# Optimization experiments

Measured on AMD Instinct MI355X. Metric: run time of the kernel, lower is better.

## Reference

```python
import jax, jax.numpy as jnp
import numpy as np

KH, KW = 3, 3
STRIDE = (1, 1)


def setup_inputs() -> dict:
    key = jax.random.key(0)
    k1, k2, k3 = jax.random.split(key, 3)
    N, C, H, W = 16, 128, 64, 64
    O = 128
    x = jax.random.normal(k1, (N, C, H, W), dtype=jnp.float32)
    # Flat weight layout [O, C*KH*KW], matching torch reshape of [O,C,KH,KW]
    weight = jax.random.normal(k2, (O, C * KH * KW), dtype=jnp.float32) * 0.02
    bias = jax.random.normal(k3, (O, 1), dtype=jnp.float32) * 0.02
    return {"x": x, "weight": weight, "bias": bias}


def reference(x, weight, bias):
    O = weight.shape[0]
    C = x.shape[1]
    # [O, C*KH*KW] -> [O, C, KH, KW]; flattening order (C major, then kh, kw)
    # matches the module's unfold/permute im2col layout.
    w4 = weight.reshape(O, C, KH, KW)
    out = jax.lax.conv_general_dilated(
        x, w4,
        window_strides=STRIDE,
        padding='VALID',
        dimension_numbers=('NCHW', 'OIHW', 'NCHW'),
    )
    return out + bias.reshape(1, O, 1, 1)
```

## Files before the change

kernel.cpp:

```cpp
#include <hip/hip_runtime.h>
#include <stdint.h>

#define AS_G __attribute__((address_space(1)))
#define AS_L __attribute__((address_space(3)))

typedef __bf16 bf16x8 __attribute__((ext_vector_type(8)));
typedef float  f32x4  __attribute__((ext_vector_type(4)));

static constexpr int NIMG = 16, CIN = 128, H = 64, W = 64, OCH = 128;
static constexpr int HO = 62, WO = 62;
static constexpr int PIX = HO * WO;
static constexpr int M_TOT = NIMG * PIX;
static constexpr int K_TOT = CIN * 9;
static constexpr int BM = 64, BK = 64;
static constexpr int KSTEPS = K_TOT / BK;
static constexpr int NWG = M_TOT / BM;
static constexpr int SLOT = 24576;
static constexpr int LDS_BYTES = 3 * SLOT;

__device__ __forceinline__ unsigned short f2bf(float f) {
    union { float f; uint32_t u; } v; v.f = f;
    uint32_t u = v.u;
    return (unsigned short)((u + 0x7FFFu + ((u >> 16) & 1u)) >> 16);
}

__global__ __launch_bounds__(256) void prep_kernel(const float* __restrict__ x,
                                                   const float* __restrict__ wsrc,
                                                   unsigned short* __restrict__ xt,
                                                   unsigned short* __restrict__ bpd) {
    __shared__ float lds[CIN][W + 4];
    if (blockIdx.x < NIMG * H) {
        const int n   = blockIdx.x >> 6;
        const int h   = blockIdx.x & 63;
        const int tid = threadIdx.x;
        {
            const int c  = tid >> 1;
            const int w0 = (tid & 1) * 32;
            const float* src = x + (((size_t)(n * CIN + c) * H + h) * W + w0);
            #pragma unroll
            for (int j = 0; j < 8; ++j) {
                float4 v = *reinterpret_cast<const float4*>(src + j * 4);
                *reinterpret_cast<float4*>(&lds[c][w0 + j * 4]) = v;
            }
        }
        __syncthreads();
        {
            const int w  = tid >> 2;
            const int c0 = (tid & 3) * 32;
            unsigned short* dst = xt + (((size_t)(n * H + h) * W + w) * CIN + c0);
            uint32_t pk[16];
            #pragma unroll
            for (int j = 0; j < 16; ++j) {
                uint32_t lo = f2bf(lds[c0 + 2 * j][w]);
                uint32_t hi = f2bf(lds[c0 + 2 * j + 1][w]);
                pk[j] = lo | (hi << 16);
            }
            #pragma unroll
            for (int j = 0; j < 4; ++j) {
                *reinterpret_cast<uint4*>(dst + j * 8) =
                    make_uint4(pk[4 * j], pk[4 * j + 1], pk[4 * j + 2], pk[4 * j + 3]);
            }
        }
    } else {
        int tid = (blockIdx.x - NIMG * H) * 256 + threadIdx.x;
        if (tid < OCH * K_TOT) {
            int o  = tid / K_TOT;
            int kp = tid - o * K_TOT;
            int t  = kp >> 7;
            int c  = kp & 127;
            bpd[tid] = f2bf(wsrc[o * K_TOT + c * 9 + t]);
        }
    }
}

__global__ __launch_bounds__(256) void gemm_kernel(const unsigned short* __restrict__ xt,
                                                   const unsigned short* __restrict__ bp,
                                                   const float* __restrict__ bias,
                                                   float* __restrict__ out) {
    extern __shared__ char lds[];
    const int tid  = threadIdx.x;
    const int wv   = tid >> 6;
    const int lane = tid & 63;

    const int orig = blockIdx.x;
    const int xcd  = orig & 7;
    const int idx  = orig >> 3;
    const int wg   = (xcd == 0 ? 0 : 121 + (xcd - 1) * 120) + idx;
    const int m0   = wg * BM;

    const int csel = ((lane & 7) ^ (lane >> 3)) * 8;
    int aBase[2], bBase[4];
    #pragma unroll
    for (int i = 0; i < 2; ++i) {
        int row = (wv * 2 + i) * 8 + (lane >> 3);
        int m = m0 + row;
        int n  = m / PIX;
        int r  = m - n * PIX;
        int y  = r / WO;
        int xx = r - y * WO;
        aBase[i] = ((n * H + y) * W + xx) * CIN;
    }
    #pragma unroll
    for (int i = 0; i < 4; ++i)
        bBase[i] = ((wv * 4 + i) * 8 + (lane >> 3)) * K_TOT;

    auto stage = [&](char* dst, int step) {
        const int t  = step >> 1;
        const int c0 = (step & 1) * 64;
        const int tapoff = (t / 3) * (W * CIN) + (t % 3) * CIN + c0;
        const int kb = step * BK;
        #pragma unroll
        for (int i = 0; i < 2; ++i)
            __builtin_amdgcn_global_load_lds(
                (AS_G unsigned int*)(xt + aBase[i] + tapoff + csel),
                (AS_L unsigned int*)(dst + (wv * 2 + i) * 1024), 16, 0, 0);
        #pragma unroll
        for (int i = 0; i < 4; ++i)
            __builtin_amdgcn_global_load_lds(
                (AS_G unsigned int*)(bp + bBase[i] + kb + csel),
                (AS_L unsigned int*)(dst + 8192 + (wv * 4 + i) * 1024), 16, 0, 0);
    };

    const int wr = wv >> 1, wc = wv & 1;
    const int lr = lane & 15, lq = lane >> 4;
    const int aRow = (wr * 32 + lr) * 128;
    const int bRow = (wc * 64 + lr) * 128;
    int colx[2];
    #pragma unroll
    for (int ks = 0; ks < 2; ++ks)
        colx[ks] = (ks * 64 + lq * 16) ^ ((lane & 7) << 4);

    f32x4 acc[2][4];
    #pragma unroll
    for (int a = 0; a < 2; ++a)
        #pragma unroll
        for (int b = 0; b < 4; ++b)
            acc[a][b] = (f32x4){0.f, 0.f, 0.f, 0.f};

    auto compute = [&](const char* base) {
        #pragma unroll
        for (int ks = 0; ks < 2; ++ks) {
            bf16x8 af[2], bfr[4];
            #pragma unroll
            for (int mi = 0; mi < 2; ++mi)
                af[mi] = *(const bf16x8*)(base + aRow + mi * 2048 + colx[ks]);
            #pragma unroll
            for (int ni = 0; ni < 4; ++ni)
                bfr[ni] = *(const bf16x8*)(base + 8192 + bRow + ni * 2048 + colx[ks]);
            __builtin_amdgcn_s_setprio(1);
            #pragma unroll
            for (int mi = 0; mi < 2; ++mi)
                #pragma unroll
                for (int ni = 0; ni < 4; ++ni)
                    acc[mi][ni] = __builtin_amdgcn_mfma_f32_16x16x32_bf16(
                        bfr[ni], af[mi], acc[mi][ni], 0, 0, 0);
            __builtin_amdgcn_s_setprio(0);
        }
    };

    char* b0 = lds;
    char* b1 = lds + SLOT;
    char* b2 = lds + 2 * SLOT;
    stage(b0, 0);
    stage(b1, 1);
    for (int t = 0; t < KSTEPS - 2; ++t) {
        stage(b2, t + 2);
        asm volatile("s_waitcnt vmcnt(12)" ::: "memory");
        __builtin_amdgcn_s_barrier();
        __builtin_amdgcn_sched_barrier(0);
        compute(b0);
        asm volatile("s_waitcnt lgkmcnt(0)" ::: "memory");
        __builtin_amdgcn_s_barrier();
        __builtin_amdgcn_sched_barrier(0);
        char* tmp = b0; b0 = b1; b1 = b2; b2 = tmp;
    }
    asm volatile("s_waitcnt vmcnt(6)" ::: "memory");
    __builtin_amdgcn_s_barrier();
    __builtin_amdgcn_sched_barrier(0);
    compute(b0);
    asm volatile("s_waitcnt vmcnt(0)" ::: "memory");
    __builtin_amdgcn_s_barrier();
    __builtin_amdgcn_sched_barrier(0);
    compute(b1);

    f32x4 bv[4];
    #pragma unroll
    for (int ni = 0; ni < 4; ++ni)
        bv[ni] = *(const f32x4*)(bias + wc * 64 + ni * 16 + lq * 4);
    #pragma unroll
    for (int mi = 0; mi < 2; ++mi) {
        int m = m0 + wr * 32 + mi * 16 + lr;
        int n  = m / PIX;
        int r  = m - n * PIX;
        int y  = r / WO;
        int xx = r - y * WO;
        float* ob = out + (size_t)n * OCH * PIX + y * WO + xx;
        #pragma unroll
        for (int ni = 0; ni < 4; ++ni)
            #pragma unroll
            for (int j = 0; j < 4; ++j) {
                int o = wc * 64 + ni * 16 + lq * 4 + j;
                ob[(size_t)o * PIX] = acc[mi][ni][j] + bv[ni][j];
            }
    }
}

extern "C" void kernel_launch(void* const* d_in, const int* in_sizes, int n_in,
                              void* d_out, int out_size, void* d_ws, size_t ws_size,
                              hipStream_t stream) {
    const float* x    = (const float*)d_in[0];
    const float* wsrc = (const float*)d_in[1];
    const float* bias = (const float*)d_in[2];
    float* out = (float*)d_out;
    unsigned short* xt = (unsigned short*)d_ws;
    unsigned short* bp = xt + (size_t)NIMG * H * W * CIN;
    prep_kernel<<<dim3(NIMG * H + (OCH * K_TOT + 255) / 256), dim3(256), 0, stream>>>(
        x, wsrc, xt, bp);
    gemm_kernel<<<dim3(NWG), dim3(256), LDS_BYTES, stream>>>(xt, bp, bias, out);
}
```

Baseline: 44.29 us.

## Enlarge GEMM block tile to 256 rows with 512 threads per block

Grows the implicit-GEMM M tile from 64 to 256 pixels and the block from 4 to 8 waves, giving each wave a 64x64 output tile (4x4 MFMA accumulators). Weight tiles staged into LDS are now reused across four times as many pixels, and each LDS fragment read feeds more MFMAs. It adds bounds clamping for the partial last tile and rebalances the XCD block remap for 241 blocks. The cost is one large block per CU with a bigger LDS footprint, fewer total blocks than CUs, and more accumulator registers per wave.

```diff
diff --git a/kernel.cpp b/kernel.cpp
--- a/kernel.cpp
+++ b/kernel.cpp
@@ -12,10 +12,12 @@
 static constexpr int PIX = HO * WO;
 static constexpr int M_TOT = NIMG * PIX;
 static constexpr int K_TOT = CIN * 9;
-static constexpr int BM = 64, BK = 64;
+static constexpr int BM = 256, BK = 64;
 static constexpr int KSTEPS = K_TOT / BK;
-static constexpr int NWG = M_TOT / BM;
-static constexpr int SLOT = 24576;
+static constexpr int NWG = (M_TOT + BM - 1) / BM;
+static constexpr int ASZ = BM * BK * 2;
+static constexpr int BSZ = OCH * BK * 2;
+static constexpr int SLOT = ASZ + BSZ;
 static constexpr int LDS_BYTES = 3 * SLOT;
 
 __device__ __forceinline__ unsigned short f2bf(float f) {
@@ -73,10 +75,10 @@
     }
 }
 
-__global__ __launch_bounds__(256) void gemm_kernel(const unsigned short* __restrict__ xt,
-                                                   const unsigned short* __restrict__ bp,
-                                                   const float* __restrict__ bias,
-                                                   float* __restrict__ out) {
+__global__ __launch_bounds__(512, 1) void gemm_kernel(const unsigned short* __restrict__ xt,
+                                                      const unsigned short* __restrict__ bp,
+                                                      const float* __restrict__ bias,
+                                                      float* __restrict__ out) {
     extern __shared__ char lds[];
     const int tid  = threadIdx.x;
     const int wv   = tid >> 6;
@@ -85,24 +87,25 @@
     const int orig = blockIdx.x;
     const int xcd  = orig & 7;
     const int idx  = orig >> 3;
-    const int wg   = (xcd == 0 ? 0 : 121 + (xcd - 1) * 120) + idx;
+    const int wg   = (xcd == 0 ? 0 : 31 + (xcd - 1) * 30) + idx;
     const int m0   = wg * BM;
 
-    const int csel = ((lane & 7) ^ (lane >> 3)) * 8;
-    int aBase[2], bBase[4];
-    #pragma unroll
-    for (int i = 0; i < 2; ++i) {
-        int row = (wv * 2 + i) * 8 + (lane >> 3);
-        int m = m0 + row;
+    const int csel = ((tid & 7) ^ ((tid >> 3) & 7)) * 8;
+    int aBase[4];
+    #pragma unroll
+    for (int p = 0; p < 4; ++p) {
+        int row = p * 64 + (tid >> 3);
+        int m = m0 + row; if (m >= M_TOT) m = M_TOT - 1;
         int n  = m / PIX;
         int r  = m - n * PIX;
         int y  = r / WO;
         int xx = r - y * WO;
-        aBase[i] = ((n * H + y) * W + xx) * CIN;
-    }
-    #pragma unroll
-    for (int i = 0; i < 4; ++i)
-        bBase[i] = ((wv * 4 + i) * 8 + (lane >> 3)) * K_TOT;
+        aBase[p] = ((n * H + y) * W + xx) * CIN;
+    }
+    int bBase[2];
+    #pragma unroll
+    for (int p = 0; p < 2; ++p)
+        bBase[p] = (p * 64 + (tid >> 3)) * K_TOT;
 
     auto stage = [&](char* dst, int step) {
         const int t  = step >> 1;
@@ -110,29 +113,29 @@
         const int tapoff = (t / 3) * (W * CIN) + (t % 3) * CIN + c0;
         const int kb = step * BK;
         #pragma unroll
-        for (int i = 0; i < 2; ++i)
+        for (int p = 0; p < 4; ++p)
             __builtin_amdgcn_global_load_lds(
-                (AS_G unsigned int*)(xt + aBase[i] + tapoff + csel),
-                (AS_L unsigned int*)(dst + (wv * 2 + i) * 1024), 16, 0, 0);
-        #pragma unroll
-        for (int i = 0; i < 4; ++i)
+                (AS_G unsigned int*)(xt + aBase[p] + tapoff + csel),
+                (AS_L unsigned int*)(dst + p * 8192 + wv * 1024), 16, 0, 0);
+        #pragma unroll
+        for (int p = 0; p < 2; ++p)
             __builtin_amdgcn_global_load_lds(
-                (AS_G unsigned int*)(bp + bBase[i] + kb + csel),
-                (AS_L unsigned int*)(dst + 8192 + (wv * 4 + i) * 1024), 16, 0, 0);
+                (AS_G unsigned int*)(bp + bBase[p] + kb + csel),
+                (AS_L unsigned int*)(dst + ASZ + p * 8192 + wv * 1024), 16, 0, 0);
     };
 
     const int wr = wv >> 1, wc = wv & 1;
     const int lr = lane & 15, lq = lane >> 4;
-    const int aRow = (wr * 32 + lr) * 128;
-    const int bRow = (wc * 64 + lr) * 128;
+    const int aRow = (wr * 64 + lr) * 128;
+    const int bRow = ASZ + (wc * 64 + lr) * 128;
     int colx[2];
     #pragma unroll
     for (int ks = 0; ks < 2; ++ks)
         colx[ks] = (ks * 64 + lq * 16) ^ ((lane & 7) << 4);
 
-    f32x4 acc[2][4];
-    #pragma unroll
-    for (int a = 0; a < 2; ++a)
+    f32x4 acc[4][4];
+    #pragma unroll
+    for (int a = 0; a < 4; ++a)
         #pragma unroll
         for (int b = 0; b < 4; ++b)
             acc[a][b] = (f32x4){0.f, 0.f, 0.f, 0.f};
@@ -140,16 +143,16 @@
     auto compute = [&](const char* base) {
         #pragma unroll
         for (int ks = 0; ks < 2; ++ks) {
-            bf16x8 af[2], bfr[4];
-            #pragma unroll
-            for (int mi = 0; mi < 2; ++mi)
+            bf16x8 af[4], bfr[4];
+            #pragma unroll
+            for (int mi = 0; mi < 4; ++mi)
                 af[mi] = *(const bf16x8*)(base + aRow + mi * 2048 + colx[ks]);
             #pragma unroll
             for (int ni = 0; ni < 4; ++ni)
-                bfr[ni] = *(const bf16x8*)(base + 8192 + bRow + ni * 2048 + colx[ks]);
+                bfr[ni] = *(const bf16x8*)(base + bRow + ni * 2048 + colx[ks]);
             __builtin_amdgcn_s_setprio(1);
             #pragma unroll
-            for (int mi = 0; mi < 2; ++mi)
+            for (int mi = 0; mi < 4; ++mi)
                 #pragma unroll
                 for (int ni = 0; ni < 4; ++ni)
                     acc[mi][ni] = __builtin_amdgcn_mfma_f32_16x16x32_bf16(
@@ -188,20 +191,22 @@
     for (int ni = 0; ni < 4; ++ni)
         bv[ni] = *(const f32x4*)(bias + wc * 64 + ni * 16 + lq * 4);
     #pragma unroll
-    for (int mi = 0; mi < 2; ++mi) {
-        int m = m0 + wr * 32 + mi * 16 + lr;
-        int n  = m / PIX;
-        int r  = m - n * PIX;
-        int y  = r / WO;
-        int xx = r - y * WO;
-        float* ob = out + (size_t)n * OCH * PIX + y * WO + xx;
-        #pragma unroll
-        for (int ni = 0; ni < 4; ++ni)
-            #pragma unroll
-            for (int j = 0; j < 4; ++j) {
-                int o = wc * 64 + ni * 16 + lq * 4 + j;
-                ob[(size_t)o * PIX] = acc[mi][ni][j] + bv[ni][j];
-            }
+    for (int mi = 0; mi < 4; ++mi) {
+        int m = m0 + wr * 64 + mi * 16 + lr;
+        if (m < M_TOT) {
+            int n  = m / PIX;
+            int r  = m - n * PIX;
+            int y  = r / WO;
+            int xx = r - y * WO;
+            float* ob = out + (size_t)n * OCH * PIX + y * WO + xx;
+            #pragma unroll
+            for (int ni = 0; ni < 4; ++ni)
+                #pragma unroll
+                for (int j = 0; j < 4; ++j) {
+                    int o = wc * 64 + ni * 16 + lq * 4 + j;
+                    ob[(size_t)o * PIX] = acc[mi][ni][j] + bv[ni][j];
+                }
+        }
     }
 }
 
@@ -216,5 +221,5 @@
     unsigned short* bp = xt + (size_t)NIMG * H * W * CIN;
     prep_kernel<<<dim3(NIMG * H + (OCH * K_TOT + 255) / 256), dim3(256), 0, stream>>>(
         x, wsrc, xt, bp);
-    gemm_kernel<<<dim3(NWG), dim3(256), LDS_BYTES, stream>>>(xt, bp, bias, out);
-}
+    gemm_kernel<<<dim3(NWG), dim3(512), LDS_BYTES, stream>>>(xt, bp, bias, out);
+}
```

After: 47.70 us. 7.7% more time.
